# Kernel tuning notes

Hardware: AMD Instinct MI355X
Metric: run time of the kernel (lower is better)

The kernel has to match this reference:

```python
import jax, jax.numpy as jnp
import numpy as np

N_QUBITS = 7
N_LAYERS = 2
DIM = 2 ** N_QUBITS  # 128
NORM_FACTOR = 1.0


def _cnot_gather_idx(n):
    # CNOT chain (0,1),(1,2),...,(n-2,n-1) plus wraparound (n-1,0).
    # new_state[x] = old_state[idx[x]]; apply gates in reverse to arange.
    gates = [(i, i + 1) for i in range(n - 1)] + [(n - 1, 0)]
    idx = np.arange(2 ** n)
    for c, t in reversed(gates):
        cbit = 1 << (n - 1 - c)  # pennylane wire 0 = most significant bit
        tbit = 1 << (n - 1 - t)
        idx = np.where((idx & cbit) > 0, idx ^ tbit, idx)
    return jnp.asarray(idx)

CNOT_IDX = _cnot_gather_idx(N_QUBITS)


def silu(x):
    return x * jax.nn.sigmoid(x)


def cayley(A_real, A_imag):
    # Hermitianize then Cayley transform -> unitary, per layer. [L,D,D]
    A = A_real.astype(jnp.complex64) + 1j * A_imag.astype(jnp.complex64)
    A = A + jnp.conj(jnp.swapaxes(A, -1, -2))
    I = jnp.eye(DIM, dtype=A.dtype)
    return jnp.matmul(A - 1j * I, jnp.linalg.inv(A + 1j * I))


def _single_qubit_gate(theta_x, theta_y):
    # combined G = RY(theta_y) @ RX(theta_x) applied to every qubit
    cx, sx = jnp.cos(theta_x / 2), jnp.sin(theta_x / 2)
    cy, sy = jnp.cos(theta_y / 2), jnp.sin(theta_y / 2)
    RX = jnp.stack([jnp.stack([cx + 0j, -1j * sx]), jnp.stack([-1j * sx, cx + 0j])])
    RY = jnp.stack([jnp.stack([cy + 0j, -sy + 0j]), jnp.stack([sy + 0j, cy + 0j])])
    return RY @ RX


def quantum_evolve(psi, coeffs, q_mats):
    # psi: [N, DIM] complex64 normalized state vectors
    N = psi.shape[0]
    for j in range(N_LAYERS):
        psi = psi @ q_mats[j].T  # QubitUnitary: new = U @ old
        G = _single_qubit_gate(coeffs[j, 0], coeffs[j, 1])
        psi = psi.reshape((N,) + (2,) * N_QUBITS)
        for ax in range(1, N_QUBITS + 1):
            psi = jnp.moveaxis(jnp.tensordot(G, psi, axes=((1,), (ax,))), 0, ax)
        psi = psi.reshape(N, DIM)
        psi = psi[:, CNOT_IDX]  # CNOT chain is a fixed basis permutation
    return psi


def setup_inputs() -> dict:
    key = jax.random.key(0)
    ks = jax.random.split(key, 16)
    N, E = 50000, 800000
    in_nf, hid, out_nf = 128, 128, 128
    h = jax.random.normal(ks[0], (N, in_nf), dtype=jnp.float32)
    edge_index = jax.random.randint(ks[1], (2, E), 0, N)
    s = 0.05
    W_e1 = jax.random.normal(ks[2], (2 * in_nf, hid), dtype=jnp.float32) * s
    b_e1 = jnp.zeros((hid,), dtype=jnp.float32)
    W_e2 = jax.random.normal(ks[3], (hid, hid), dtype=jnp.float32) * s
    b_e2 = jnp.zeros((hid,), dtype=jnp.float32)
    W_enc = jax.random.normal(ks[4], (hid + in_nf, DIM), dtype=jnp.float32) * s
    b_enc = jnp.zeros((DIM,), dtype=jnp.float32)
    coeffs = jax.random.normal(ks[5], (N_LAYERS, 2), dtype=jnp.float32) * 0.1
    A_real = jax.random.normal(ks[6], (N_LAYERS, DIM, DIM), dtype=jnp.float32) * 0.01
    A_imag = jax.random.normal(ks[7], (N_LAYERS, DIM, DIM), dtype=jnp.float32) * 0.01
    W_dec = jax.random.normal(ks[8], (DIM, out_nf), dtype=jnp.float32) * s
    b_dec = jnp.zeros((out_nf,), dtype=jnp.float32)
    return {"h": h, "edge_index": edge_index, "W_e1": W_e1, "b_e1": b_e1,
            "W_e2": W_e2, "b_e2": b_e2, "W_enc": W_enc, "b_enc": b_enc,
            "coeffs": coeffs, "A_real": A_real, "A_imag": A_imag,
            "W_dec": W_dec, "b_dec": b_dec}


def reference(h, edge_index, W_e1, b_e1, W_e2, b_e2, W_enc, b_enc,
              coeffs, A_real, A_imag, W_dec, b_dec):
    row, col = edge_index[0], edge_index[1]
    # edge model: mij = MLP([h_src, h_tgt])
    e = jnp.concatenate([h[row], h[col]], axis=1)  # [E, 2*in_nf]
    e = silu(e @ W_e1 + b_e1)
    edge_feat = silu(e @ W_e2 + b_e2)  # [E, hid]
    # node model: scatter-sum aggregation over destination `row`
    agg = jax.ops.segment_sum(edge_feat, row, num_segments=h.shape[0]) / NORM_FACTOR
    q_input = jnp.concatenate([h, agg], axis=1) @ W_enc + b_enc  # [N, DIM]
    norm = jnp.sqrt(jnp.sum(q_input ** 2, axis=1, keepdims=True) + 1e-12)
    psi = (q_input / norm).astype(jnp.complex64)
    q_mats = cayley(A_real, A_imag)  # [L, DIM, DIM] unitary
    psi = quantum_evolve(psi, coeffs, q_mats)
    out = h + (jnp.real(psi) @ W_dec + b_dec)
    return out, edge_feat
```

## Files before the change

kernel.cpp:

```cpp
#include <hip/hip_runtime.h>
#include <math.h>

#define N_NODES 50000
#define N_EDGES 800000
#define NS_ITERS 2

typedef __attribute__((ext_vector_type(8))) short bf16x8;
typedef __attribute__((ext_vector_type(2))) short shortx2;
typedef __attribute__((ext_vector_type(4))) float f32x4;

__device__ __forceinline__ float silu_f(float x) {
    float d = 1.0f + __expf(-x);
    return x * __builtin_amdgcn_rcpf(d);
}

__device__ __forceinline__ unsigned short f2bf(float x) {
    union { float f; unsigned u; } v; v.f = x;
    unsigned r = v.u + 0x7FFFu + ((v.u >> 16) & 1u);
    return (unsigned short)(r >> 16);
}

__device__ __forceinline__ void atomic_pk_add_bf16(short* addr, shortx2 v) {
    typedef shortx2 __attribute__((address_space(1)))* gp1;
    __builtin_amdgcn_global_atomic_fadd_v2bf16((gp1)(unsigned long long)addr, v);
}

__global__ __launch_bounds__(256) void hbfcount_kernel(const float* __restrict__ h,
                                                       short* __restrict__ hbf,
                                                       const int* __restrict__ ei,
                                                       int* __restrict__ cnt) {
    int i = blockIdx.x * 256 + threadIdx.x;
    const float4* h4 = (const float4*)h;
    float4 v0 = h4[i * 2], v1 = h4[i * 2 + 1];
    bf16x8 b;
    b[0] = (short)f2bf(v0.x); b[1] = (short)f2bf(v0.y);
    b[2] = (short)f2bf(v0.z); b[3] = (short)f2bf(v0.w);
    b[4] = (short)f2bf(v1.x); b[5] = (short)f2bf(v1.y);
    b[6] = (short)f2bf(v1.z); b[7] = (short)f2bf(v1.w);
    ((bf16x8*)hbf)[i] = b;
    atomicAdd(&cnt[ei[i]], 1);
}

__global__ __launch_bounds__(1024) void scan_kernel(const int* __restrict__ cnt,
                                                    int* __restrict__ cursor) {
    __shared__ int sA[1024];
    __shared__ int sB[1024];
    const int t = threadIdx.x;
    const int CH = 49;
    int s = 0;
    #pragma unroll 4
    for (int i = 0; i < CH; ++i) {
        int idx = t * CH + i;
        if (idx < N_NODES) s += cnt[idx];
    }
    sA[t] = s;
    __syncthreads();
    int* src = sA;
    int* dst = sB;
    for (int off = 1; off < 1024; off <<= 1) {
        int v = src[t];
        if (t >= off) v += src[t - off];
        dst[t] = v;
        __syncthreads();
        int* tmp = src; src = dst; dst = tmp;
    }
    int run = (t == 0) ? 0 : src[t - 1];
    for (int i = 0; i < CH; ++i) {
        int idx = t * CH + i;
        if (idx < N_NODES) {
            cursor[idx] = run;
            run += cnt[idx];
        }
    }
}

__global__ __launch_bounds__(256) void fill_kernel(const int* __restrict__ ei,
                                                   int* __restrict__ cursor,
                                                   int* __restrict__ elist) {
    int e = blockIdx.x * 256 + threadIdx.x;
    if (e < N_EDGES) {
        int slot = atomicAdd(&cursor[ei[e]], 1);
        elist[slot] = e;
    }
}

__global__ __launch_bounds__(1024) void hmat_kernel(const float* __restrict__ A_real,
                                                    const float* __restrict__ A_imag,
                                                    float* __restrict__ H,
                                                    float* __restrict__ X) {
    const int L = blockIdx.x;
    const int t = threadIdx.x;
    const float* ar = A_real + L * 16384;
    const float* ai = A_imag + L * 16384;
    float* hre = H + L * 32768;
    float* him = hre + 16384;
    float* xre = X + L * 32768;
    float* xim = xre + 16384;
    for (int q = 0; q < 16; ++q) {
        int idx = t + 1024 * q;
        int i = idx >> 7, j = idx & 127;
        float hr = ar[idx] + ar[j * 128 + i];
        float hi = ai[idx] - ai[j * 128 + i];
        hre[idx] = hr;
        him[idx] = hi;
        xre[idx] = hr;
        xim[idx] = hi - (i == j ? 1.0f : 0.0f);
    }
}

__global__ __launch_bounds__(512) void ns_t_kernel(const float* __restrict__ H,
                                                   const float* __restrict__ X,
                                                   float* __restrict__ T) {
    const int L = blockIdx.x >> 5;
    const int t = threadIdx.x;
    const int i = (blockIdx.x & 31) * 4 + (t >> 7);
    const int j = t & 127;
    const float* hre = H + L * 32768;
    const float* him = hre + 16384;
    const float* xre = X + L * 32768;
    const float* xim = xre + 16384;
    float accr = 0.f, acci = 0.f;
    #pragma unroll 4
    for (int k = 0; k < 128; ++k) {
        float hr = hre[i * 128 + k], hi = him[i * 128 + k];
        float xr = xre[k * 128 + j], xi = xim[k * 128 + j];
        accr += hr * xr - hi * xi;
        acci += hr * xi + hi * xr;
    }
    T[L * 32768 + i * 128 + j]         = accr - xim[i * 128 + j];
    T[L * 32768 + 16384 + i * 128 + j] = acci + xre[i * 128 + j];
}

__global__ __launch_bounds__(512) void ns_x_kernel(const float* __restrict__ X,
                                                   const float* __restrict__ T,
                                                   float* __restrict__ Xout) {
    const int L = blockIdx.x >> 5;
    const int t = threadIdx.x;
    const int i = (blockIdx.x & 31) * 4 + (t >> 7);
    const int j = t & 127;
    const float* xre = X + L * 32768;
    const float* xim = xre + 16384;
    const float* tre = T + L * 32768;
    const float* tim = tre + 16384;
    float accr = 0.f, acci = 0.f;
    #pragma unroll 4
    for (int k = 0; k < 128; ++k) {
        float xr = xre[i * 128 + k], xi = xim[i * 128 + k];
        float tr = tre[k * 128 + j], ti = tim[k * 128 + j];
        accr += xr * tr - xi * ti;
        acci += xr * ti + xi * tr;
    }
    Xout[L * 32768 + i * 128 + j]         = 2.0f * xre[i * 128 + j] - accr;
    Xout[L * 32768 + 16384 + i * 128 + j] = 2.0f * xim[i * 128 + j] - acci;
}

__global__ __launch_bounds__(1024) void gateperm_kernel(const float* __restrict__ X,
                                                        const float* __restrict__ coeffs,
                                                        float* __restrict__ Y) {
    __shared__ float Mre[128 * 129];
    __shared__ float Mim[128 * 129];
    const int L = blockIdx.x;
    const int t = threadIdx.x;
    const float* xre = X + L * 32768;
    const float* xim = xre + 16384;

    for (int q = 0; q < 16; ++q) {
        int idx = t + 1024 * q;
        int i = idx >> 7, j = idx & 127;
        Mre[i * 129 + j] = (i == j ? 1.0f : 0.0f) + 2.0f * xim[idx];
        Mim[i * 129 + j] = -2.0f * xre[idx];
    }
    __syncthreads();

    const float tx = coeffs[2 * L + 0] * 0.5f;
    const float ty = coeffs[2 * L + 1] * 0.5f;
    const float cx = cosf(tx), sx = sinf(tx), cy = cosf(ty), sy = sinf(ty);
    const float G00r = cx * cy, G00i = sx * sy;
    const float G01r = -cx * sy, G01i = -sx * cy;
    const float G10r = cx * sy, G10i = -sx * cy;
    const float G11r = cx * cy, G11i = -sx * sy;

    for (int st = 0; st < 7; ++st) {
        int b = 1 << st;
        #pragma unroll
        for (int p = 0; p < 8; ++p) {
            int pid = t + 1024 * p;
            int col = pid & 127, ph = pid >> 7;
            int i0 = ((ph >> st) << (st + 1)) | (ph & (b - 1));
            int i1 = i0 | b;
            float v0r = Mre[i0 * 129 + col], v0i = Mim[i0 * 129 + col];
            float v1r = Mre[i1 * 129 + col], v1i = Mim[i1 * 129 + col];
            Mre[i0 * 129 + col] = G00r * v0r - G00i * v0i + G01r * v1r - G01i * v1i;
            Mim[i0 * 129 + col] = G00r * v0i + G00i * v0r + G01r * v1i + G01i * v1r;
            Mre[i1 * 129 + col] = G10r * v0r - G10i * v0i + G11r * v1r - G11i * v1i;
            Mim[i1 * 129 + col] = G10r * v0i + G10i * v0r + G11r * v1i + G11i * v1r;
        }
        __syncthreads();
    }

    const int cs[7] = {6, 5, 4, 3, 2, 1, 0};
    const int ts[7] = {0, 6, 5, 4, 3, 2, 1};
    float* yre = Y + L * 32768;
    float* yim = yre + 16384;
    for (int q = 0; q < 16; ++q) {
        int idx = t + 1024 * q;
        int ii_ = idx >> 7, col = idx & 127;
        int s = ii_;
        #pragma unroll
        for (int m = 0; m < 7; ++m) {
            int cbit = 1 << (6 - cs[m]);
            int tbit = 1 << (6 - ts[m]);
            if (s & cbit) s ^= tbit;
        }
        yre[idx] = Mre[s * 129 + col];
        yim[idx] = Mim[s * 129 + col];
    }
}

__global__ __launch_bounds__(512) void combine1_kernel(const float* __restrict__ Y,
                                                       float* __restrict__ ReM) {
    __shared__ float q1r[16384];
    __shared__ float q1i[16384];
    const int t = threadIdx.x;
    const float* q1re = Y;
    const float* q1im = Y + 16384;
    const float* q2re = Y + 32768;
    const float* q2im = Y + 49152;
    for (int q = 0; q < 32; ++q) {
        q1r[t + 512 * q] = q1re[t + 512 * q];
        q1i[t + 512 * q] = q1im[t + 512 * q];
    }
    __syncthreads();
    int i = blockIdx.x * 4 + (t >> 7);
    int j = t & 127;
    float acc = 0.f;
    for (int k = 0; k < 128; ++k) {
        acc += q2re[i * 128 + k] * q1r[k * 128 + j] - q2im[i * 128 + k] * q1i[k * 128 + j];
    }
    ReM[i * 128 + j] = acc;
}

__global__ __launch_bounds__(512) void combine2_kernel(const float* __restrict__ ReM,
                                                       const float* __restrict__ W_dec,
                                                       short* __restrict__ Dt) {
    __shared__ float ml[16384];
    __shared__ float wl[16384];
    const int t = threadIdx.x;
    for (int q = 0; q < 32; ++q) {
        ml[t + 512 * q] = ReM[t + 512 * q];
        wl[t + 512 * q] = W_dec[t + 512 * q];
    }
    __syncthreads();
    int k = blockIdx.x * 4 + (t >> 7);
    int j = t & 127;
    float acc = 0.f;
    for (int i = 0; i < 128; ++i) {
        acc += ml[i * 128 + k] * wl[i * 128 + j];
    }
    Dt[j * 128 + k] = (short)f2bf(acc);
}

__global__ __launch_bounds__(768)
__attribute__((amdgpu_waves_per_eu(3, 3)))
void edge_kernel(const short* __restrict__ hbf,
                 const int* __restrict__ ei,
                 const int* __restrict__ elist,
                 const float* __restrict__ W_e1,
                 const float* __restrict__ b_e1,
                 const float* __restrict__ W_e2,
                 const float* __restrict__ b_e2,
                 float* __restrict__ ef_out,
                 short* __restrict__ agg_bf) {
    __shared__ short w1t[128 * 256];
    __shared__ short w2t[128 * 128];
    __shared__ short c1s[12][1024];
    __shared__ float bias1[128];
    __shared__ float bias2[128];

    const int t = threadIdx.x;
    const int lane = t & 63;
    const int w = t >> 6;
    const int l15 = lane & 15;
    const int kg = lane >> 4;

    {
        const float4* w1_4 = (const float4*)W_e1;
        for (int idx4 = t; idx4 < 8192; idx4 += 768) {
            int k = idx4 >> 5, j4 = idx4 & 31;
            float4 v = w1_4[idx4];
            int j = j4 * 4;
            w1t[(j + 0) * 256 + (k ^ (((j + 0) & 7) << 3))] = (short)f2bf(v.x);
            w1t[(j + 1) * 256 + (k ^ (((j + 1) & 7) << 3))] = (short)f2bf(v.y);
            w1t[(j + 2) * 256 + (k ^ (((j + 2) & 7) << 3))] = (short)f2bf(v.z);
            w1t[(j + 3) * 256 + (k ^ (((j + 3) & 7) << 3))] = (short)f2bf(v.w);
        }
        const float4* w2_4 = (const float4*)W_e2;
        for (int idx4 = t; idx4 < 4096; idx4 += 768) {
            int k = idx4 >> 5, j4 = idx4 & 31;
            float4 v = w2_4[idx4];
            int j = j4 * 4;
            w2t[(j + 0) * 128 + (k ^ (((j + 0) & 7) << 3))] = (short)f2bf(v.x);
            w2t[(j + 1) * 128 + (k ^ (((j + 1) & 7) << 3))] = (short)f2bf(v.y);
            w2t[(j + 2) * 128 + (k ^ (((j + 2) & 7) << 3))] = (short)f2bf(v.z);
            w2t[(j + 3) * 128 + (k ^ (((j + 3) & 7) << 3))] = (short)f2bf(v.w);
        }
        if (t < 128) { bias1[t] = b_e1[t]; bias2[t] = b_e2[t]; }
    }
    __syncthreads();

    const bf16x8* hb8 = (const bf16x8*)hbf;
    short* myc1 = &c1s[w][0];
    const int nt = N_EDGES / 16;
    const int TW = gridDim.x * 12;
    const int wvid = blockIdx.x * 12 + w;
    int tile = (int)(((long long)nt * wvid) / TW);
    const int tend = (int)(((long long)nt * (wvid + 1)) / TW);
    if (tile >= tend) return;

    int el = elist[tile * 16 + l15];
    int ri = ei[el];
    int ci = ei[N_EDGES + el];
    bf16x8 a1[8];
    #pragma unroll
    for (int s = 0; s < 4; ++s) a1[s] = hb8[(size_t)ri * 16 + s * 4 + kg];
    #pragma unroll
    for (int s = 0; s < 4; ++s) a1[4 + s] = hb8[(size_t)ci * 16 + s * 4 + kg];

    bool hn = (tile + 1 < tend);
    int eln = 0, rin = 0, cin = 0;
    if (hn) {
        eln = elist[(tile + 1) * 16 + l15];
        rin = ei[eln];
        cin = ei[N_EDGES + eln];
    }

    float runsum[8];
    #pragma unroll
    for (int nf = 0; nf < 8; ++nf) runsum[nf] = 0.f;

    for (;;) {
        bool hn2 = (tile + 2 < tend);
        int eln2 = 0, rin2 = 0, cin2 = 0;
        if (hn2) {
            eln2 = elist[(tile + 2) * 16 + l15];
            rin2 = ei[eln2];
            cin2 = ei[N_EDGES + eln2];
        }

        f32x4 acc[8];
        #pragma unroll
        for (int nf = 0; nf < 8; ++nf) acc[nf] = (f32x4){0.f, 0.f, 0.f, 0.f};
        #pragma unroll
        for (int s = 0; s < 8; ++s) {
            const int k0 = s * 32 + kg * 8;
            #pragma unroll
            for (int nf = 0; nf < 8; ++nf) {
                int brow = nf * 16 + l15;
                bf16x8 b = *(const bf16x8*)&w1t[brow * 256 + (k0 ^ ((brow & 7) << 3))];
                acc[nf] = __builtin_amdgcn_mfma_f32_16x16x32_bf16(a1[s], b, acc[nf], 0, 0, 0);
            }
        }

        bf16x8 a1n[8];
        if (hn) {
            #pragma unroll
            for (int s = 0; s < 4; ++s) a1n[s] = hb8[(size_t)rin * 16 + s * 4 + kg];
            #pragma unroll
            for (int s = 0; s < 4; ++s) a1n[4 + s] = hb8[(size_t)cin * 16 + s * 4 + kg];
        }

        f32x4 acc2[8];
        #pragma unroll
        for (int nf = 0; nf < 8; ++nf) acc2[nf] = (f32x4){0.f, 0.f, 0.f, 0.f};
        #pragma unroll
        for (int half = 0; half < 2; ++half) {
            #pragma unroll
            for (int nfh = 0; nfh < 4; ++nfh) {
                int nf = half * 4 + nfh;
                float bj1 = bias1[nf * 16 + l15];
                #pragma unroll
                for (int r = 0; r < 4; ++r) {
                    int row = kg * 4 + r;
                    int c = nfh * 16 + l15;
                    myc1[row * 64 + (c ^ ((row & 7) << 3))] =
                        (short)f2bf(silu_f(acc[nf][r] + bj1));
                }
            }
            #pragma unroll
            for (int s2l = 0; s2l < 2; ++s2l) {
                int k0h = s2l * 32 + kg * 8;
                bf16x8 a2 = *(const bf16x8*)&myc1[l15 * 64 + (k0h ^ ((l15 & 7) << 3))];
                int k0g = half * 64 + k0h;
                #pragma unroll
                for (int nf = 0; nf < 8; ++nf) {
                    int brow = nf * 16 + l15;
                    bf16x8 b = *(const bf16x8*)&w2t[brow * 128 + (k0g ^ ((brow & 7) << 3))];
                    acc2[nf] = __builtin_amdgcn_mfma_f32_16x16x32_bf16(a2, b, acc2[nf], 0, 0, 0);
                }
            }
        }

        int rw[4], ew[4];
        #pragma unroll
        for (int r = 0; r < 4; ++r) {
            rw[r] = __shfl(ri, kg * 4 + r);
            ew[r] = __shfl(el, kg * 4 + r);
        }
        int rwn0 = hn ? __shfl(rin, kg * 4) : -1;
        #pragma unroll
        for (int r = 0; r < 4; ++r) {
            float* efp = ef_out + (size_t)ew[r] * 128;
            #pragma unroll
            for (int nf = 0; nf < 8; ++nf) {
                int col = nf * 16 + l15;
                float v = silu_f(acc2[nf][r] + bias2[col]);
                __builtin_nontemporal_store(v, efp + col);
                runsum[nf] += v;
            }
            bool end = (r < 3) ? (rw[r + 1] != rw[r]) : (rw[3] != rwn0);
            if (end) {
                short* agp = agg_bf + (size_t)rw[r] * 128;
                #pragma unroll
                for (int nf = 0; nf < 8; ++nf) {
                    float vn = __shfl_xor(runsum[nf], 1);
                    if ((l15 & 1) == 0) {
                        shortx2 pk;
                        pk.x = (short)f2bf(runsum[nf]);
                        pk.y = (short)f2bf(vn);
                        atomic_pk_add_bf16(agp + nf * 16 + l15, pk);
                    }
                    runsum[nf] = 0.f;
                }
            }
        }

        if (!hn) break;
        tile += 1;
        el = eln; ri = rin; ci = cin;
        #pragma unroll
        for (int s = 0; s < 8; ++s) a1[s] = a1n[s];
        hn = hn2; eln = eln2; rin = rin2; cin = cin2;
    }
}

__global__ __launch_bounds__(1024)
__attribute__((amdgpu_waves_per_eu(4, 4)))
void node_kernel(const short* __restrict__ hbf,
                 const short* __restrict__ agg_bf,
                 const float* __restrict__ W_enc,
                 const float* __restrict__ b_enc,
                 const short* __restrict__ Dt_bf,
                 const float* __restrict__ b_dec,
                 const float* __restrict__ h,
                 float* __restrict__ out) {
    __shared__ short wet[128 * 256];
    __shared__ short dtl[128 * 128];
    __shared__ short c1s[16][1024];

    const int t = threadIdx.x;
    const int lane = t & 63;
    const int w = t >> 6;
    const int l15 = lane & 15;
    const int kg = lane >> 4;

    {
        const float4* we4 = (const float4*)W_enc;
        for (int q = 0; q < 8; ++q) {
            int idx4 = t + 1024 * q;
            int k = idx4 >> 5, j4 = idx4 & 31;
            float4 v = we4[idx4];
            int j = j4 * 4;
            wet[(j + 0) * 256 + (k ^ (((j + 0) & 7) << 3))] = (short)f2bf(v.x);
            wet[(j + 1) * 256 + (k ^ (((j + 1) & 7) << 3))] = (short)f2bf(v.y);
            wet[(j + 2) * 256 + (k ^ (((j + 2) & 7) << 3))] = (short)f2bf(v.z);
            wet[(j + 3) * 256 + (k ^ (((j + 3) & 7) << 3))] = (short)f2bf(v.w);
        }
        const int4* s4 = (const int4*)Dt_bf;
        for (int q = 0; q < 2; ++q) {
            int idx4 = t + 1024 * q;
            int j = idx4 >> 4, c = idx4 & 15;
            int k0 = c * 8;
            int4 v = s4[idx4];
            *(int4*)&dtl[j * 128 + (k0 ^ ((j & 7) << 3))] = v;
        }
    }
    float bj1[8], bj2[8];
    #pragma unroll
    for (int nf = 0; nf < 8; ++nf) {
        bj1[nf] = b_enc[nf * 16 + l15];
        bj2[nf] = b_dec[nf * 16 + l15];
    }
    __syncthreads();

    const bf16x8* hb8 = (const bf16x8*)hbf;
    const bf16x8* ab8 = (const bf16x8*)agg_bf;
    short* myc1 = &c1s[w][0];
    const int nt = N_NODES / 16;
    const int tile = blockIdx.x * 16 + w;
    if (tile >= nt) return;

    const int node = tile * 16 + l15;
    bf16x8 a[8];
    #pragma unroll
    for (int s = 0; s < 4; ++s) a[s] = hb8[(size_t)node * 16 + s * 4 + kg];
    #pragma unroll
    for (int s = 0; s < 4; ++s) a[4 + s] = ab8[(size_t)node * 16 + s * 4 + kg];

    f32x4 acc[8];
    #pragma unroll
    for (int nf = 0; nf < 8; ++nf) acc[nf] = (f32x4){0.f, 0.f, 0.f, 0.f};
    #pragma unroll
    for (int s = 0; s < 8; ++s) {
        const int k0 = s * 32 + kg * 8;
        #pragma unroll
        for (int nf = 0; nf < 8; ++nf) {
            int brow = nf * 16 + l15;
            bf16x8 b = *(const bf16x8*)&wet[brow * 256 + (k0 ^ ((brow & 7) << 3))];
            acc[nf] = __builtin_amdgcn_mfma_f32_16x16x32_bf16(a[s], b, acc[nf], 0, 0, 0);
        }
    }

    float nr[4] = {0.f, 0.f, 0.f, 0.f};
    #pragma unroll
    for (int nf = 0; nf < 8; ++nf) {
        #pragma unroll
        for (int r = 0; r < 4; ++r) {
            acc[nf][r] += bj1[nf];
            nr[r] += acc[nf][r] * acc[nf][r];
        }
    }
    #pragma unroll
    for (int r = 0; r < 4; ++r) {
        nr[r] += __shfl_xor(nr[r], 1);
        nr[r] += __shfl_xor(nr[r], 2);
        nr[r] += __shfl_xor(nr[r], 4);
        nr[r] += __shfl_xor(nr[r], 8);
        nr[r] = 1.0f / sqrtf(nr[r] + 1e-12f);
    }

    f32x4 acc2[8];
    #pragma unroll
    for (int nf = 0; nf < 8; ++nf) acc2[nf] = (f32x4){0.f, 0.f, 0.f, 0.f};
    #pragma unroll
    for (int half = 0; half < 2; ++half) {
        #pragma unroll
        for (int nfh = 0; nfh < 4; ++nfh) {
            int nf = half * 4 + nfh;
            #pragma unroll
            for (int r = 0; r < 4; ++r) {
                int row = kg * 4 + r;
                int c = nfh * 16 + l15;
                myc1[row * 64 + (c ^ ((row & 7) << 3))] = (short)f2bf(acc[nf][r] * nr[r]);
            }
        }
        #pragma unroll
        for (int s2l = 0; s2l < 2; ++s2l) {
            int k0h = s2l * 32 + kg * 8;
            bf16x8 a2 = *(const bf16x8*)&myc1[l15 * 64 + (k0h ^ ((l15 & 7) << 3))];
            int k0g = half * 64 + k0h;
            #pragma unroll
            for (int nf = 0; nf < 8; ++nf) {
                int brow = nf * 16 + l15;
                bf16x8 b = *(const bf16x8*)&dtl[brow * 128 + (k0g ^ ((brow & 7) << 3))];
                acc2[nf] = __builtin_amdgcn_mfma_f32_16x16x32_bf16(a2, b, acc2[nf], 0, 0, 0);
            }
        }
    }

    #pragma unroll
    for (int r = 0; r < 4; ++r) {
        size_t rowb = (size_t)(tile * 16 + kg * 4 + r) * 128;
        #pragma unroll
        for (int nf = 0; nf < 8; ++nf) {
            int col = nf * 16 + l15;
            out[rowb + col] = h[rowb + col] + acc2[nf][r] + bj2[nf];
        }
    }
}

extern "C" void kernel_launch(void* const* d_in, const int* in_sizes, int n_in,
                              void* d_out, int out_size, void* d_ws, size_t ws_size,
                              hipStream_t stream) {
    const float* h      = (const float*)d_in[0];
    const int*   ei     = (const int*)d_in[1];
    const float* W_e1   = (const float*)d_in[2];
    const float* b_e1   = (const float*)d_in[3];
    const float* W_e2   = (const float*)d_in[4];
    const float* b_e2   = (const float*)d_in[5];
    const float* W_enc  = (const float*)d_in[6];
    const float* b_enc  = (const float*)d_in[7];
    const float* coeffs = (const float*)d_in[8];
    const float* A_real = (const float*)d_in[9];
    const float* A_imag = (const float*)d_in[10];
    const float* W_dec  = (const float*)d_in[11];
    const float* b_dec  = (const float*)d_in[12];

    float* out    = (float*)d_out;
    float* ef_out = out + (size_t)N_NODES * 128;

    short* agg_bf = (short*)d_ws;
    short* h_bf   = agg_bf + (size_t)N_NODES * 128;
    int*   cnt    = (int*)(h_bf + (size_t)N_NODES * 128);
    int*   cursor = cnt + 50176;
    int*   elist  = cursor + 50176;
    float* small  = (float*)(elist + N_EDGES);
    float* Ybuf   = small;
    float* ReM    = Ybuf + 65536;
    float* Hbuf   = ReM + 16384;
    float* Xa     = Hbuf + 65536;
    float* Xb     = Xa + 65536;
    float* Tbuf   = Xb + 65536;
    short* Dt_bf  = (short*)(Tbuf + 65536);

    hipMemsetAsync(agg_bf, 0, (size_t)N_NODES * 128 * sizeof(short), stream);
    hipMemsetAsync(cnt, 0, 50176 * sizeof(int), stream);

    hbfcount_kernel<<<3125, 256, 0, stream>>>(h, h_bf, ei, cnt);
    scan_kernel<<<1, 1024, 0, stream>>>(cnt, cursor);
    fill_kernel<<<3125, 256, 0, stream>>>(ei, cursor, elist);

    hmat_kernel<<<2, 1024, 0, stream>>>(A_real, A_imag, Hbuf, Xa);
    float* xc = Xa;
    float* xn = Xb;
    for (int it = 0; it < NS_ITERS; ++it) {
        ns_t_kernel<<<64, 512, 0, stream>>>(Hbuf, xc, Tbuf);
        ns_x_kernel<<<64, 512, 0, stream>>>(xc, Tbuf, xn);
        float* tmp = xc; xc = xn; xn = tmp;
    }
    gateperm_kernel<<<2, 1024, 0, stream>>>(xc, coeffs, Ybuf);
    combine1_kernel<<<32, 512, 0, stream>>>(Ybuf, ReM);
    combine2_kernel<<<32, 512, 0, stream>>>(ReM, W_dec, Dt_bf);

    edge_kernel<<<256, 768, 0, stream>>>(h_bf, ei, elist, W_e1, b_e1, W_e2, b_e2,
                                         ef_out, agg_bf);

    node_kernel<<<196, 1024, 0, stream>>>(h_bf, agg_bf, W_enc, b_enc, Dt_bf, b_dec, h, out);
}
```

Baseline: 624.3 us.

## Merge preprocessing and Newton-Schulz launches, reorder edge loads, pad LDS layout

Fuses the bf16 conversion, edge counting and Hermitian matrix setup into one launch. The scan is packed with the first Newton-Schulz step, and the edge fill with the second, which cuts the launch count and merges two memsets into one. In the edge kernel, biases move into registers, the next-edge gathers are issued earlier to overlap with the first MFMA stage, and the XOR-swizzled intermediate buffer becomes a padded 68-stride layout read with two 4-wide loads. These trade extra register pressure and a possibly less conflict-free LDS pattern for fewer launches and more latency hiding.

Result: faster. 604.7 us (-3.1%).

```diff
diff --git a/kernel.cpp b/kernel.cpp
--- a/kernel.cpp
+++ b/kernel.cpp
@@ -3,9 +3,9 @@
 
 #define N_NODES 50000
 #define N_EDGES 800000
-#define NS_ITERS 2
 
 typedef __attribute__((ext_vector_type(8))) short bf16x8;
+typedef __attribute__((ext_vector_type(4))) short bf16x4;
 typedef __attribute__((ext_vector_type(2))) short shortx2;
 typedef __attribute__((ext_vector_type(4))) float f32x4;
 
@@ -25,95 +25,55 @@
     __builtin_amdgcn_global_atomic_fadd_v2bf16((gp1)(unsigned long long)addr, v);
 }
 
-__global__ __launch_bounds__(256) void hbfcount_kernel(const float* __restrict__ h,
-                                                       short* __restrict__ hbf,
-                                                       const int* __restrict__ ei,
-                                                       int* __restrict__ cnt) {
-    int i = blockIdx.x * 256 + threadIdx.x;
-    const float4* h4 = (const float4*)h;
-    float4 v0 = h4[i * 2], v1 = h4[i * 2 + 1];
-    bf16x8 b;
-    b[0] = (short)f2bf(v0.x); b[1] = (short)f2bf(v0.y);
-    b[2] = (short)f2bf(v0.z); b[3] = (short)f2bf(v0.w);
-    b[4] = (short)f2bf(v1.x); b[5] = (short)f2bf(v1.y);
-    b[6] = (short)f2bf(v1.z); b[7] = (short)f2bf(v1.w);
-    ((bf16x8*)hbf)[i] = b;
-    atomicAdd(&cnt[ei[i]], 1);
-}
-
-__global__ __launch_bounds__(1024) void scan_kernel(const int* __restrict__ cnt,
-                                                    int* __restrict__ cursor) {
-    __shared__ int sA[1024];
-    __shared__ int sB[1024];
-    const int t = threadIdx.x;
-    const int CH = 49;
-    int s = 0;
-    #pragma unroll 4
-    for (int i = 0; i < CH; ++i) {
-        int idx = t * CH + i;
-        if (idx < N_NODES) s += cnt[idx];
-    }
-    sA[t] = s;
-    __syncthreads();
-    int* src = sA;
-    int* dst = sB;
-    for (int off = 1; off < 1024; off <<= 1) {
-        int v = src[t];
-        if (t >= off) v += src[t - off];
-        dst[t] = v;
-        __syncthreads();
-        int* tmp = src; src = dst; dst = tmp;
-    }
-    int run = (t == 0) ? 0 : src[t - 1];
-    for (int i = 0; i < CH; ++i) {
-        int idx = t * CH + i;
-        if (idx < N_NODES) {
-            cursor[idx] = run;
-            run += cnt[idx];
-        }
-    }
-}
-
-__global__ __launch_bounds__(256) void fill_kernel(const int* __restrict__ ei,
-                                                   int* __restrict__ cursor,
-                                                   int* __restrict__ elist) {
-    int e = blockIdx.x * 256 + threadIdx.x;
-    if (e < N_EDGES) {
-        int slot = atomicAdd(&cursor[ei[e]], 1);
-        elist[slot] = e;
-    }
-}
-
-__global__ __launch_bounds__(1024) void hmat_kernel(const float* __restrict__ A_real,
-                                                    const float* __restrict__ A_imag,
-                                                    float* __restrict__ H,
-                                                    float* __restrict__ X) {
-    const int L = blockIdx.x;
-    const int t = threadIdx.x;
-    const float* ar = A_real + L * 16384;
-    const float* ai = A_imag + L * 16384;
-    float* hre = H + L * 32768;
-    float* him = hre + 16384;
-    float* xre = X + L * 32768;
-    float* xim = xre + 16384;
-    for (int q = 0; q < 16; ++q) {
-        int idx = t + 1024 * q;
-        int i = idx >> 7, j = idx & 127;
-        float hr = ar[idx] + ar[j * 128 + i];
-        float hi = ai[idx] - ai[j * 128 + i];
-        hre[idx] = hr;
-        him[idx] = hi;
-        xre[idx] = hr;
-        xim[idx] = hi - (i == j ? 1.0f : 0.0f);
-    }
-}
-
-__global__ __launch_bounds__(512) void ns_t_kernel(const float* __restrict__ H,
-                                                   const float* __restrict__ X,
-                                                   float* __restrict__ T) {
-    const int L = blockIdx.x >> 5;
-    const int t = threadIdx.x;
-    const int i = (blockIdx.x & 31) * 4 + (t >> 7);
+__global__ __launch_bounds__(256) void prep_kernel(const float* __restrict__ h,
+                                                   short* __restrict__ hbf,
+                                                   const int* __restrict__ ei,
+                                                   int* __restrict__ cnt,
+                                                   const float* __restrict__ A_real,
+                                                   const float* __restrict__ A_imag,
+                                                   float* __restrict__ H,
+                                                   float* __restrict__ X) {
+    const int bid = blockIdx.x;
+    const int t = threadIdx.x;
+    if (bid < 3125) {
+        int i = bid * 256 + t;
+        const float4* h4 = (const float4*)h;
+        float4 v0 = h4[i * 2], v1 = h4[i * 2 + 1];
+        bf16x8 b;
+        b[0] = (short)f2bf(v0.x); b[1] = (short)f2bf(v0.y);
+        b[2] = (short)f2bf(v0.z); b[3] = (short)f2bf(v0.w);
+        b[4] = (short)f2bf(v1.x); b[5] = (short)f2bf(v1.y);
+        b[6] = (short)f2bf(v1.z); b[7] = (short)f2bf(v1.w);
+        ((bf16x8*)hbf)[i] = b;
+        atomicAdd(&cnt[ei[i]], 1);
+    } else {
+        int p = bid - 3125;
+        int L = p >> 2, q4 = p & 3;
+        const float* ar = A_real + L * 16384;
+        const float* ai = A_imag + L * 16384;
+        float* hre = H + L * 32768;
+        float* him = hre + 16384;
+        float* xre = X + L * 32768;
+        float* xim = xre + 16384;
+        for (int m = 0; m < 16; ++m) {
+            int idx = q4 * 4096 + t + 256 * m;
+            int i = idx >> 7, j = idx & 127;
+            float hr = ar[idx] + ar[j * 128 + i];
+            float hi = ai[idx] - ai[j * 128 + i];
+            hre[idx] = hr;
+            him[idx] = hi;
+            xre[idx] = hr;
+            xim[idx] = hi - (i == j ? 1.0f : 0.0f);
+        }
+    }
+}
+
+__device__ __forceinline__ void ns_t_body(int blk, int t,
+                                          const float* __restrict__ H,
+                                          const float* __restrict__ X,
+                                          float* __restrict__ T) {
+    const int L = blk >> 4;
+    const int i = (blk & 15) * 8 + (t >> 7);
     const int j = t & 127;
     const float* hre = H + L * 32768;
     const float* him = hre + 16384;
@@ -127,16 +87,16 @@
         accr += hr * xr - hi * xi;
         acci += hr * xi + hi * xr;
     }
-    T[L * 32768 + i * 128 + j]         = accr - xim[i * 128 + j];
-    T[L * 32768 + 16384 + i * 128 + j] = acci + xre[i * 128 + j];
-}
-
-__global__ __launch_bounds__(512) void ns_x_kernel(const float* __restrict__ X,
-                                                   const float* __restrict__ T,
-                                                   float* __restrict__ Xout) {
-    const int L = blockIdx.x >> 5;
-    const int t = threadIdx.x;
-    const int i = (blockIdx.x & 31) * 4 + (t >> 7);
+    T[L * 32768 + i * 128 + j]          = accr - xim[i * 128 + j];
+    T[L * 32768 + 16384 + i * 128 + j]  = acci + xre[i * 128 + j];
+}
+
+__device__ __forceinline__ void ns_x_body(int blk, int t,
+                                          const float* __restrict__ X,
+                                          const float* __restrict__ T,
+                                          float* __restrict__ Xout) {
+    const int L = blk >> 4;
+    const int i = (blk & 15) * 8 + (t >> 7);
     const int j = t & 127;
     const float* xre = X + L * 32768;
     const float* xim = xre + 16384;
@@ -150,8 +110,77 @@
         accr += xr * tr - xi * ti;
         acci += xr * ti + xi * tr;
     }
-    Xout[L * 32768 + i * 128 + j]         = 2.0f * xre[i * 128 + j] - accr;
-    Xout[L * 32768 + 16384 + i * 128 + j] = 2.0f * xim[i * 128 + j] - acci;
+    Xout[L * 32768 + i * 128 + j]          = 2.0f * xre[i * 128 + j] - accr;
+    Xout[L * 32768 + 16384 + i * 128 + j]  = 2.0f * xim[i * 128 + j] - acci;
+}
+
+__global__ __launch_bounds__(1024) void nst_scan_kernel(const float* __restrict__ H,
+                                                        const float* __restrict__ X,
+                                                        float* __restrict__ T,
+                                                        const int* __restrict__ cnt,
+                                                        int* __restrict__ cursor) {
+    const int bid = blockIdx.x;
+    const int t = threadIdx.x;
+    if (bid < 32) { ns_t_body(bid, t, H, X, T); return; }
+    __shared__ int sA[1024];
+    __shared__ int sB[1024];
+    const int CH = 49;
+    int s = 0;
+    #pragma unroll 4
+    for (int i = 0; i < CH; ++i) {
+        int idx = t * CH + i;
+        if (idx < N_NODES) s += cnt[idx];
+    }
+    sA[t] = s;
+    __syncthreads();
+    int* src = sA;
+    int* dst = sB;
+    for (int off = 1; off < 1024; off <<= 1) {
+        int v = src[t];
+        if (t >= off) v += src[t - off];
+        dst[t] = v;
+        __syncthreads();
+        int* tmp = src; src = dst; dst = tmp;
+    }
+    int run = (t == 0) ? 0 : src[t - 1];
+    for (int i = 0; i < CH; ++i) {
+        int idx = t * CH + i;
+        if (idx < N_NODES) {
+            cursor[idx] = run;
+            run += cnt[idx];
+        }
+    }
+}
+
+__global__ __launch_bounds__(1024) void fill_nsx_kernel(const int* __restrict__ ei,
+                                                        int* __restrict__ cursor,
+                                                        int* __restrict__ elist,
+                                                        const float* __restrict__ X,
+                                                        const float* __restrict__ T,
+                                                        float* __restrict__ Xout) {
+    const int bid = blockIdx.x;
+    const int t = threadIdx.x;
+    if (bid < 782) {
+        int e = bid * 1024 + t;
+        if (e < N_EDGES) {
+            int slot = atomicAdd(&cursor[ei[e]], 1);
+            elist[slot] = e;
+        }
+        return;
+    }
+    ns_x_body(bid - 782, t, X, T, Xout);
+}
+
+__global__ __launch_bounds__(1024) void ns_t_kernel(const float* __restrict__ H,
+                                                    const float* __restrict__ X,
+                                                    float* __restrict__ T) {
+    ns_t_body(blockIdx.x, threadIdx.x, H, X, T);
+}
+
+__global__ __launch_bounds__(1024) void ns_x_kernel(const float* __restrict__ X,
+                                                    const float* __restrict__ T,
+                                                    float* __restrict__ Xout) {
+    ns_x_body(blockIdx.x, threadIdx.x, X, T, Xout);
 }
 
 __global__ __launch_bounds__(1024) void gateperm_kernel(const float* __restrict__ X,
@@ -273,9 +302,7 @@
                  short* __restrict__ agg_bf) {
     __shared__ short w1t[128 * 256];
     __shared__ short w2t[128 * 128];
-    __shared__ short c1s[12][1024];
-    __shared__ float bias1[128];
-    __shared__ float bias2[128];
+    __shared__ short c1s[12][16 * 68];
 
     const int t = threadIdx.x;
     const int lane = t & 63;
@@ -304,7 +331,12 @@
             w2t[(j + 2) * 128 + (k ^ (((j + 2) & 7) << 3))] = (short)f2bf(v.z);
             w2t[(j + 3) * 128 + (k ^ (((j + 3) & 7) << 3))] = (short)f2bf(v.w);
         }
-        if (t < 128) { bias1[t] = b_e1[t]; bias2[t] = b_e2[t]; }
+    }
+    float b1v[8], b2v[8];
+    #pragma unroll
+    for (int nf = 0; nf < 8; ++nf) {
+        b1v[nf] = b_e1[nf * 16 + l15];
+        b2v[nf] = b_e2[nf * 16 + l15];
     }
     __syncthreads();
 
@@ -347,6 +379,14 @@
             cin2 = ei[N_EDGES + eln2];
         }
 
+        bf16x8 a1n[8];
+        if (hn) {
+            #pragma unroll
+            for (int s = 0; s < 4; ++s) a1n[s] = hb8[(size_t)rin * 16 + s * 4 + kg];
+            #pragma unroll
+            for (int s = 0; s < 4; ++s) a1n[4 + s] = hb8[(size_t)cin * 16 + s * 4 + kg];
+        }
+
         f32x4 acc[8];
         #pragma unroll
         for (int nf = 0; nf < 8; ++nf) acc[nf] = (f32x4){0.f, 0.f, 0.f, 0.f};
@@ -361,14 +401,6 @@
             }
         }
 
-        bf16x8 a1n[8];
-        if (hn) {
-            #pragma unroll
-            for (int s = 0; s < 4; ++s) a1n[s] = hb8[(size_t)rin * 16 + s * 4 + kg];
-            #pragma unroll
-            for (int s = 0; s < 4; ++s) a1n[4 + s] = hb8[(size_t)cin * 16 + s * 4 + kg];
-        }
-
         f32x4 acc2[8];
         #pragma unroll
         for (int nf = 0; nf < 8; ++nf) acc2[nf] = (f32x4){0.f, 0.f, 0.f, 0.f};
@@ -377,19 +409,22 @@
             #pragma unroll
             for (int nfh = 0; nfh < 4; ++nfh) {
                 int nf = half * 4 + nfh;
-                float bj1 = bias1[nf * 16 + l15];
                 #pragma unroll
                 for (int r = 0; r < 4; ++r) {
                     int row = kg * 4 + r;
                     int c = nfh * 16 + l15;
-                    myc1[row * 64 + (c ^ ((row & 7) << 3))] =
-                        (short)f2bf(silu_f(acc[nf][r] + bj1));
+                    myc1[row * 68 + c] = (short)f2bf(silu_f(acc[nf][r] + b1v[nf]));
                 }
             }
             #pragma unroll
             for (int s2l = 0; s2l < 2; ++s2l) {
                 int k0h = s2l * 32 + kg * 8;
-                bf16x8 a2 = *(const bf16x8*)&myc1[l15 * 64 + (k0h ^ ((l15 & 7) << 3))];
+                int base = l15 * 68 + k0h;
+                bf16x4 lo = *(const bf16x4*)&myc1[base];
+                bf16x4 hi = *(const bf16x4*)&myc1[base + 4];
+                bf16x8 a2;
+                #pragma unroll
+                for (int z = 0; z < 4; ++z) { a2[z] = lo[z]; a2[4 + z] = hi[z]; }
                 int k0g = half * 64 + k0h;
                 #pragma unroll
                 for (int nf = 0; nf < 8; ++nf) {
@@ -413,7 +448,7 @@
             #pragma unroll
             for (int nf = 0; nf < 8; ++nf) {
                 int col = nf * 16 + l15;
-                float v = silu_f(acc2[nf][r] + bias2[col]);
+                float v = silu_f(acc2[nf][r] + b2v[nf]);
                 __builtin_nontemporal_store(v, efp + col);
                 runsum[nf] += v;
             }
@@ -599,9 +634,9 @@
     float* ef_out = out + (size_t)N_NODES * 128;
 
     short* agg_bf = (short*)d_ws;
-    short* h_bf   = agg_bf + (size_t)N_NODES * 128;
-    int*   cnt    = (int*)(h_bf + (size_t)N_NODES * 128);
-    int*   cursor = cnt + 50176;
+    int*   cnt    = (int*)(agg_bf + (size_t)N_NODES * 128);
+    short* h_bf   = (short*)(cnt + 50176);
+    int*   cursor = (int*)(h_bf + (size_t)N_NODES * 128);
     int*   elist  = cursor + 50176;
     float* small  = (float*)(elist + N_EDGES);
     float* Ybuf   = small;
@@ -612,22 +647,16 @@
     float* Tbuf   = Xb + 65536;
     short* Dt_bf  = (short*)(Tbuf + 65536);
 
-    hipMemsetAsync(agg_bf, 0, (size_t)N_NODES * 128 * sizeof(short), stream);
-    hipMemsetAsync(cnt, 0, 50176 * sizeof(int), stream);
-
-    hbfcount_kernel<<<3125, 256, 0, stream>>>(h, h_bf, ei, cnt);
-    scan_kernel<<<1, 1024, 0, stream>>>(cnt, cursor);
-    fill_kernel<<<3125, 256, 0, stream>>>(ei, cursor, elist);
-
-    hmat_kernel<<<2, 1024, 0, stream>>>(A_real, A_imag, Hbuf, Xa);
-    float* xc = Xa;
-    float* xn = Xb;
-    for (int it = 0; it < NS_ITERS; ++it) {
-        ns_t_kernel<<<64, 512, 0, stream>>>(Hbuf, xc, Tbuf);
-        ns_x_kernel<<<64, 512, 0, stream>>>(xc, Tbuf, xn);
-        float* tmp = xc; xc = xn; xn = tmp;
-    }
-    gateperm_kernel<<<2, 1024, 0, stream>>>(xc, coeffs, Ybuf);
+    hipMemsetAsync(agg_bf, 0, (size_t)N_NODES * 128 * sizeof(short) + 50176 * sizeof(int),
+                   stream);
+
+    prep_kernel<<<3133, 256, 0, stream>>>(h, h_bf, ei, cnt, A_real, A_imag, Hbuf, Xa);
+    nst_scan_kernel<<<33, 1024, 0, stream>>>(Hbuf, Xa, Tbuf, cnt, cursor);
+    fill_nsx_kernel<<<814, 1024, 0, stream>>>(ei, cursor, elist, Xa, Tbuf, Xb);
+    ns_t_kernel<<<32, 1024, 0, stream>>>(Hbuf, Xb, Tbuf);
+    ns_x_kernel<<<32, 1024, 0, stream>>>(Xb, Tbuf, Xa);
+
+    gateperm_kernel<<<2, 1024, 0, stream>>>(Xa, coeffs, Ybuf);
     combine1_kernel<<<32, 512, 0, stream>>>(Ybuf, ReM);
     combine2_kernel<<<32, 512, 0, stream>>>(ReM, W_dec, Dt_bf);
 
```
